# Kernel optimization log

Measured on AMD Instinct MI355X. Metric: run time of the kernel, lower is better.

## Reference

```python
import jax, jax.numpy as jnp
import numpy as np
import math

HIDDEN = 1024

def setup_inputs() -> dict:
    key = jax.random.key(0)
    k1, k2, k3, k4, k5 = jax.random.split(key, 5)
    s = 1.0 / math.sqrt(HIDDEN)
    return {
        "x": jax.random.normal(k1, (4, 2048, HIDDEN), dtype=jnp.float32),
        "W_qkv": jax.random.uniform(k2, (HIDDEN, 3 * HIDDEN), jnp.float32, -s, s),
        "b_qkv": jax.random.uniform(k3, (3 * HIDDEN,), jnp.float32, -s, s),
        "W_out": jax.random.uniform(k4, (HIDDEN, HIDDEN), jnp.float32, -s, s),
        "b_out": jax.random.uniform(k5, (HIDDEN,), jnp.float32, -s, s),
    }

def reference(x, W_qkv, b_qkv, W_out, b_out):
    # fused QKV projection: [b, s, 3h]
    qkv = jnp.einsum("bsh,hd->bsd", x, W_qkv) + b_qkv
    q, k, v = jnp.split(qkv, 3, axis=-1)
    scale = 1.0 / math.sqrt(x.shape[-1])
    scores = jnp.einsum("bqh,bkh->bqk", q, k) * scale  # [b, s, s]
    attn = jax.nn.softmax(scores, axis=-1)
    out = jnp.einsum("bqk,bkh->bqh", attn, v)
    return jnp.einsum("bsh,hd->bsd", out, W_out) + b_out
```

## Files before the change

kernel.cpp:

```cpp
#include <hip/hip_runtime.h>
#include <cstdint>
#include <cstddef>


typedef __bf16 bf16;
typedef __bf16 bf16x8 __attribute__((ext_vector_type(8)));
typedef __bf16 bf16x4 __attribute__((ext_vector_type(4)));
typedef float  f32x4  __attribute__((ext_vector_type(4)));

#define THREADS 512
#define BM 256
#define BN 128
#define BK 64
#define UNIT 8192
#define BUFELS (3*UNIT)
#define NBUF 3

__device__ __forceinline__ void gload_lds16(const bf16* g, bf16* l) {
  __builtin_amdgcn_global_load_lds(
      (const __attribute__((address_space(1))) unsigned int*)g,
      (__attribute__((address_space(3))) unsigned int*)l,
      16, 0, 0);
}

__device__ __forceinline__ void stage_unit(const bf16* g0, long ld, bf16* ldsu, int tid) {
  const int wv = tid >> 6;
  #pragma unroll
  for (int j = 0; j < 2; ++j) {
    const int c = j * 512 + tid;
    const int r = c >> 3;
    const int sg = (c & 7) ^ (r & 7);
    const int cb = j * 512 + (wv << 6);
    gload_lds16(g0 + (long)r * ld + sg * 8, ldsu + (size_t)cb * 8);
  }
}

__device__ __forceinline__ bf16x8 rd_frag(const bf16* unitb, int r, int s) {
  return *(const bf16x8*)(unitb + (size_t)r * 64 + (size_t)((s ^ (r & 7)) * 8));
}

template <int MODE>
__device__ __forceinline__ void gemm_body(
    const bf16* __restrict__ A, long sAz, int lda,
    const bf16* __restrict__ B, long sBz, int ldb, int K,
    bf16* __restrict__ p0, long sCz,
    bf16* __restrict__ p1, bf16* __restrict__ p2,
    float* __restrict__ fout, const float* __restrict__ bias, float scale) {
  __shared__ bf16 lds[NBUF * BUFELS];
  const int tid = threadIdx.x;
  const int wv = tid >> 6, ln = tid & 63;
  const int wr = wv >> 1, wc = wv & 1;
  const int lr = ln & 15, lh = ln >> 4;
  const int m0 = blockIdx.x * BM, n0 = blockIdx.y * BN;
  const int z = blockIdx.z;
  A += (long)z * sAz;
  B += (long)z * sBz;
  const bf16* Ag = A + (long)m0 * lda;
  const bf16* Bg = B + (long)n0 * ldb;
  const int NT = K / BK;

  #pragma unroll
  for (int t = 0; t < 2; ++t) {
    bf16* bb = lds + t * BUFELS;
    stage_unit(Ag + t * BK, lda, bb, tid);
    stage_unit(Ag + (long)128 * lda + t * BK, lda, bb + UNIT, tid);
    stage_unit(Bg + t * BK, ldb, bb + 2 * UNIT, tid);
  }
  asm volatile("s_waitcnt vmcnt(6)" ::: "memory");
  __builtin_amdgcn_sched_barrier(0);
  __builtin_amdgcn_s_barrier();

  f32x4 acc[4][4];
  #pragma unroll
  for (int i = 0; i < 4; ++i)
    #pragma unroll
    for (int j = 0; j < 4; ++j)
      acc[i][j] = f32x4{0.f, 0.f, 0.f, 0.f};

  const int aru = (wr & 1) * 64;
  const int au  = wr >> 1;

  int buf = 0, nb = 2;
  for (int t = 0; t < NT; ++t) {
    const bf16* Au = lds + buf * BUFELS + au * UNIT;
    const bf16* Bu = lds + buf * BUFELS + 2 * UNIT;
    bf16* Pn = lds + nb * BUFELS;
    const bool pf = (t + 2 < NT);
    bf16x8 aF[2][2], bF[4][2];

    #pragma unroll
    for (int i = 0; i < 2; ++i)
      #pragma unroll
      for (int ks = 0; ks < 2; ++ks)
        aF[i][ks] = rd_frag(Au, aru + i * 16 + lr, (ks << 2) + lh);
    #pragma unroll
    for (int nf = 0; nf < 4; ++nf)
      #pragma unroll
      for (int ks = 0; ks < 2; ++ks)
        bF[nf][ks] = rd_frag(Bu, wc * 64 + nf * 16 + lr, (ks << 2) + lh);
    if (pf) {
      stage_unit(Ag + (long)(t + 2) * BK, lda, Pn, tid);
      stage_unit(Ag + (long)128 * lda + (long)(t + 2) * BK, lda, Pn + UNIT, tid);
    }
    __builtin_amdgcn_s_barrier();
    asm volatile("s_waitcnt lgkmcnt(0)" ::: "memory");
    __builtin_amdgcn_sched_barrier(0);
    __builtin_amdgcn_s_setprio(1);
    #pragma unroll
    for (int i = 0; i < 2; ++i)
      #pragma unroll
      for (int nf = 0; nf < 4; ++nf)
        #pragma unroll
        for (int ks = 0; ks < 2; ++ks)
          acc[i][nf] = __builtin_amdgcn_mfma_f32_16x16x32_bf16(aF[i][ks], bF[nf][ks], acc[i][nf], 0, 0, 0);
    __builtin_amdgcn_s_setprio(0);
    __builtin_amdgcn_s_barrier();

    #pragma unroll
    for (int i = 0; i < 2; ++i)
      #pragma unroll
      for (int ks = 0; ks < 2; ++ks)
        aF[i][ks] = rd_frag(Au, aru + 32 + i * 16 + lr, (ks << 2) + lh);
    if (pf) stage_unit(Bg + (long)(t + 2) * BK, ldb, Pn + 2 * UNIT, tid);
    __builtin_amdgcn_s_barrier();
    asm volatile("s_waitcnt lgkmcnt(0)" ::: "memory");
    __builtin_amdgcn_sched_barrier(0);
    __builtin_amdgcn_s_setprio(1);
    #pragma unroll
    for (int i = 0; i < 2; ++i)
      #pragma unroll
      for (int nf = 0; nf < 4; ++nf)
        #pragma unroll
        for (int ks = 0; ks < 2; ++ks)
          acc[2 + i][nf] = __builtin_amdgcn_mfma_f32_16x16x32_bf16(aF[i][ks], bF[nf][ks], acc[2 + i][nf], 0, 0, 0);
    __builtin_amdgcn_s_setprio(0);
    if (t + 1 < NT) {
      if (pf) asm volatile("s_waitcnt vmcnt(6)" ::: "memory");
      else    asm volatile("s_waitcnt vmcnt(0)" ::: "memory");
      __builtin_amdgcn_sched_barrier(0);
    }
    __builtin_amdgcn_s_barrier();

    buf = (buf == 2) ? 0 : buf + 1;
    nb  = (nb == 2) ? 0 : nb + 1;
  }

  #pragma unroll
  for (int mf = 0; mf < 4; ++mf) {
    #pragma unroll
    for (int nf = 0; nf < 4; ++nf) {
      #pragma unroll
      for (int rg = 0; rg < 4; ++rg) {
        const int gm = m0 + wr * 64 + mf * 16 + lh * 4 + rg;
        const int gn = n0 + wc * 64 + nf * 16 + lr;
        float v = acc[mf][nf][rg];
        if constexpr (MODE == 0) {
          v += bias[gn];
          if (gn < 1024)       p0[(size_t)gm * 1024 + gn] = (bf16)v;
          else if (gn < 2048)  p1[(size_t)gm * 1024 + (gn - 1024)] = (bf16)v;
          else                 p2[(size_t)gm * 1024 + (gn - 2048)] = (bf16)v;
        } else if constexpr (MODE == 1) {
          p0[(size_t)z * sCz + (size_t)gm * 2048 + gn] = (bf16)(v * scale);
        } else if constexpr (MODE == 2) {
          p0[(size_t)z * sCz + (size_t)gm * 1024 + gn] = (bf16)v;
        } else {
          fout[(size_t)gm * 1024 + gn] = v + bias[gn];
        }
      }
    }
  }
}

#define GEMM_ARGS const bf16* A, long sAz, int lda, const bf16* B, long sBz, int ldb, \
                  int K, bf16* p0, long sCz, bf16* p1, bf16* p2, float* fout,         \
                  const float* bias, float scale
__global__ __launch_bounds__(THREADS, 2) void gemm_qkv(GEMM_ARGS) {
  gemm_body<0>(A, sAz, lda, B, sBz, ldb, K, p0, sCz, p1, p2, fout, bias, scale);
}
__global__ __launch_bounds__(THREADS, 2) void gemm_sc(GEMM_ARGS) {
  gemm_body<1>(A, sAz, lda, B, sBz, ldb, K, p0, sCz, p1, p2, fout, bias, scale);
}
__global__ __launch_bounds__(THREADS, 2) void gemm_pv(GEMM_ARGS) {
  gemm_body<2>(A, sAz, lda, B, sBz, ldb, K, p0, sCz, p1, p2, fout, bias, scale);
}
__global__ __launch_bounds__(THREADS, 2) void gemm_out(GEMM_ARGS) {
  gemm_body<3>(A, sAz, lda, B, sBz, ldb, K, p0, sCz, p1, p2, fout, bias, scale);
}

__global__ __launch_bounds__(256) void k_f32_to_bf16(const float* __restrict__ in,
                                                     bf16* __restrict__ out, long n) {
  long i = ((long)blockIdx.x * blockDim.x + threadIdx.x) * 4;
  if (i + 3 < n) {
    float4 v = *(const float4*)(in + i);
    bf16x4 o;
    o[0] = (bf16)v.x; o[1] = (bf16)v.y; o[2] = (bf16)v.z; o[3] = (bf16)v.w;
    *(bf16x4*)(out + i) = o;
  }
}

__global__ __launch_bounds__(256) void k_transpose(const float* __restrict__ in,
                                                   bf16* __restrict__ out, int R, int C) {
  __shared__ float t[32][33];
  int c0 = blockIdx.x * 32, r0 = blockIdx.y * 32;
  int tx = threadIdx.x, ty = threadIdx.y;
  #pragma unroll
  for (int dy = 0; dy < 32; dy += 8)
    t[ty + dy][tx] = in[(size_t)(r0 + ty + dy) * C + c0 + tx];
  __syncthreads();
  #pragma unroll
  for (int dy = 0; dy < 32; dy += 8)
    out[(size_t)(c0 + ty + dy) * R + r0 + tx] = (bf16)t[tx][ty + dy];
}

__global__ __launch_bounds__(256) void k_transpose_v(const bf16* __restrict__ in,
                                                     bf16* __restrict__ out) {
  __shared__ bf16 t[32][33];
  const int z = blockIdx.z;
  in  += (size_t)z * 2048 * 1024;
  out += (size_t)z * 1024 * 2048;
  int h0 = blockIdx.x * 32, s0 = blockIdx.y * 32;
  int tx = threadIdx.x, ty = threadIdx.y;
  #pragma unroll
  for (int dy = 0; dy < 32; dy += 8)
    t[ty + dy][tx] = in[(size_t)(s0 + ty + dy) * 1024 + h0 + tx];
  __syncthreads();
  #pragma unroll
  for (int dy = 0; dy < 32; dy += 8)
    out[(size_t)(h0 + ty + dy) * 2048 + s0 + tx] = t[tx][ty + dy];
}

__global__ __launch_bounds__(256) void k_softmax(bf16* __restrict__ S) {
  const int row = blockIdx.x;
  bf16* p = S + (size_t)row * 2048;
  const int tid = threadIdx.x;
  bf16x8 vin = *(const bf16x8*)(p + tid * 8);
  float x[8];
  float mx = -1e30f;
  #pragma unroll
  for (int i = 0; i < 8; ++i) { x[i] = (float)vin[i]; mx = fmaxf(mx, x[i]); }
  #pragma unroll
  for (int off = 32; off; off >>= 1) mx = fmaxf(mx, __shfl_down(mx, off));
  __shared__ float redm[4];
  if ((tid & 63) == 0) redm[tid >> 6] = mx;
  __syncthreads();
  mx = fmaxf(fmaxf(redm[0], redm[1]), fmaxf(redm[2], redm[3]));
  float s = 0.f;
  #pragma unroll
  for (int i = 0; i < 8; ++i) { x[i] = __expf(x[i] - mx); s += x[i]; }
  #pragma unroll
  for (int off = 32; off; off >>= 1) s += __shfl_down(s, off);
  __shared__ float reds[4];
  if ((tid & 63) == 0) reds[tid >> 6] = s;
  __syncthreads();
  s = reds[0] + reds[1] + reds[2] + reds[3];
  float inv = 1.0f / s;
  bf16x8 vo;
  #pragma unroll
  for (int i = 0; i < 8; ++i) vo[i] = (bf16)(x[i] * inv);
  *(bf16x8*)(p + tid * 8) = vo;
}

extern "C" void kernel_launch(void* const* d_in, const int* in_sizes, int n_in,
                              void* d_out, int out_size, void* d_ws, size_t ws_size,
                              hipStream_t stream) {
  const float* x    = (const float*)d_in[0];
  const float* Wqkv = (const float*)d_in[1];
  const float* bqkv = (const float*)d_in[2];
  const float* Wout = (const float*)d_in[3];
  const float* bout = (const float*)d_in[4];
  float* out = (float*)d_out;

  char* w = (char*)d_ws;
  const size_t MB = 1ull << 20;
  bf16* Xb  = (bf16*)(w);
  bf16* WqT = (bf16*)(w + 16 * MB);
  bf16* WoT = (bf16*)(w + 22 * MB);
  bf16* Qb  = (bf16*)(w + 24 * MB);
  bf16* Kb  = (bf16*)(w + 40 * MB);
  bf16* Vb  = (bf16*)(w + 56 * MB);
  bf16* Sb  = (bf16*)(w + 72 * MB);
  bf16* AO  = (bf16*)(w + 104 * MB);
  bf16* VT  = Xb;

  k_f32_to_bf16<<<8192, 256, 0, stream>>>(x, Xb, 8388608L);
  dim3 tb(32, 8);
  k_transpose<<<dim3(96, 32), tb, 0, stream>>>(Wqkv, WqT, 1024, 3072);
  k_transpose<<<dim3(32, 32), tb, 0, stream>>>(Wout, WoT, 1024, 1024);

  gemm_qkv<<<dim3(32, 24), THREADS, 0, stream>>>(
      Xb, 0L, 1024, WqT, 0L, 1024, 1024, Qb, 0L, Kb, Vb, nullptr, bqkv, 1.0f);

  k_transpose_v<<<dim3(32, 64, 4), tb, 0, stream>>>(Vb, VT);

  gemm_sc<<<dim3(8, 16, 4), THREADS, 0, stream>>>(
      Qb, 2048L * 1024, 1024, Kb, 2048L * 1024, 1024, 1024,
      Sb, 2048L * 2048, nullptr, nullptr, nullptr, nullptr, 0.03125f);

  k_softmax<<<8192, 256, 0, stream>>>(Sb);

  gemm_pv<<<dim3(8, 8, 4), THREADS, 0, stream>>>(
      Sb, 2048L * 2048, 2048, VT, 1024L * 2048, 2048, 2048,
      AO, 2048L * 1024, nullptr, nullptr, nullptr, nullptr, 1.0f);

  gemm_out<<<dim3(32, 8), THREADS, 0, stream>>>(
      AO, 0L, 1024, WoT, 0L, 1024, 1024,
      nullptr, 0L, nullptr, nullptr, out, bout, 1.0f);
}
```

Before: 227.2 us.

## Use 256x256 GEMM tiles with 8-phase double-buffered pipeline and XCD block swizzle

Grows the shared GEMM tile from 256x128 to 256x256 with a 2x4 wave layout and a 32-fragment accumulator per wave. The K loop becomes eight phases over two 64-wide LDS buffers, each quarter-unit prefetch staged between fragment reads and MFMAs with tuned vmcnt gates. Blocks are remapped with a stride-8 swizzle so neighbouring tiles land on the same XCD. The aim is more data reuse per LDS load and better L2 locality, at the cost of more registers, fewer blocks (worse wave fill on small grids like gemm_out) and fragile wait-count bookkeeping.

```diff
diff --git a/kernel.cpp b/kernel.cpp
--- a/kernel.cpp
+++ b/kernel.cpp
@@ -10,17 +10,13 @@
 
 #define THREADS 512
 #define BM 256
-#define BN 128
-#define BK 64
+#define BN 256
 #define UNIT 8192
-#define BUFELS (3*UNIT)
-#define NBUF 3
 
 __device__ __forceinline__ void gload_lds16(const bf16* g, bf16* l) {
   __builtin_amdgcn_global_load_lds(
       (const __attribute__((address_space(1))) unsigned int*)g,
-      (__attribute__((address_space(3))) unsigned int*)l,
-      16, 0, 0);
+      (__attribute__((address_space(3))) unsigned int*)l, 16, 0, 0);
 }
 
 __device__ __forceinline__ void stage_unit(const bf16* g0, long ld, bf16* ldsu, int tid) {
@@ -39,121 +35,120 @@
   return *(const bf16x8*)(unitb + (size_t)r * 64 + (size_t)((s ^ (r & 7)) * 8));
 }
 
+#define GATE(N)  asm volatile("s_waitcnt vmcnt(" #N ")" ::: "memory")
+#define LGKM0()  asm volatile("s_waitcnt lgkmcnt(0)" ::: "memory")
+#define SBAR()   __builtin_amdgcn_s_barrier()
+#define SCHED0() __builtin_amdgcn_sched_barrier(0)
+
+#define PHASE(DB, MH, NH, RA, RB, STAGE_CODE, GATE_CODE)                         \
+  {                                                                              \
+    if (RA) {                                                                    \
+      _Pragma("unroll") for (int mf = 0; mf < 4; ++mf)                           \
+        _Pragma("unroll") for (int ks = 0; ks < 2; ++ks)                         \
+          aF[mf][ks] = rd_frag(&lds[DB][MH][0], wsm * 64 + mf * 16 + lr, ks * 4 + lh); \
+    }                                                                            \
+    if (RB) {                                                                    \
+      _Pragma("unroll") for (int nf = 0; nf < 2; ++nf)                           \
+        _Pragma("unroll") for (int ks = 0; ks < 2; ++ks)                         \
+          bF[NH][nf][ks] = rd_frag(&lds[DB][2 + NH][0], wsn * 32 + nf * 16 + lr, ks * 4 + lh); \
+    }                                                                            \
+    STAGE_CODE;                                                                  \
+    SBAR();                                                                      \
+    LGKM0();                                                                     \
+    SCHED0();                                                                    \
+    __builtin_amdgcn_s_setprio(1);                                               \
+    _Pragma("unroll") for (int mf = 0; mf < 4; ++mf)                             \
+      _Pragma("unroll") for (int nf = 0; nf < 2; ++nf)                           \
+        _Pragma("unroll") for (int ks = 0; ks < 2; ++ks)                         \
+          acc[(MH)*4 + mf][(NH)*2 + nf] = __builtin_amdgcn_mfma_f32_16x16x32_bf16( \
+              aF[mf][ks], bF[NH][nf][ks], acc[(MH)*4 + mf][(NH)*2 + nf], 0, 0, 0); \
+    __builtin_amdgcn_s_setprio(0);                                               \
+    GATE_CODE;                                                                   \
+    SBAR();                                                                      \
+    SCHED0();                                                                    \
+  }
+
 template <int MODE>
 __device__ __forceinline__ void gemm_body(
     const bf16* __restrict__ A, long sAz, int lda,
     const bf16* __restrict__ B, long sBz, int ldb, int K,
-    bf16* __restrict__ p0, long sCz,
-    bf16* __restrict__ p1, bf16* __restrict__ p2,
+    bf16* __restrict__ p0, long sCz, bf16* __restrict__ p1, bf16* __restrict__ p2,
     float* __restrict__ fout, const float* __restrict__ bias, float scale) {
-  __shared__ bf16 lds[NBUF * BUFELS];
+  __shared__ bf16 lds[2][4][UNIT];
   const int tid = threadIdx.x;
   const int wv = tid >> 6, ln = tid & 63;
-  const int wr = wv >> 1, wc = wv & 1;
+  const int wsm = wv >> 2, wsn = wv & 3;
   const int lr = ln & 15, lh = ln >> 4;
-  const int m0 = blockIdx.x * BM, n0 = blockIdx.y * BN;
-  const int z = blockIdx.z;
-  A += (long)z * sAz;
-  B += (long)z * sBz;
-  const bf16* Ag = A + (long)m0 * lda;
-  const bf16* Bg = B + (long)n0 * ldb;
-  const int NT = K / BK;
-
-  #pragma unroll
-  for (int t = 0; t < 2; ++t) {
-    bf16* bb = lds + t * BUFELS;
-    stage_unit(Ag + t * BK, lda, bb, tid);
-    stage_unit(Ag + (long)128 * lda + t * BK, lda, bb + UNIT, tid);
-    stage_unit(Bg + t * BK, ldb, bb + 2 * UNIT, tid);
-  }
-  asm volatile("s_waitcnt vmcnt(6)" ::: "memory");
-  __builtin_amdgcn_sched_barrier(0);
-  __builtin_amdgcn_s_barrier();
-
-  f32x4 acc[4][4];
-  #pragma unroll
-  for (int i = 0; i < 4; ++i)
+
+  const int gx = gridDim.x, gy = gridDim.y;
+  const int lin = blockIdx.x + gx * (blockIdx.y + gy * blockIdx.z);
+  const int nwg = gx * gy * gridDim.z;
+  const int swz = (lin & 7) * (nwg >> 3) + (lin >> 3);
+  const int bx = swz % gx;
+  const int tq = swz / gx;
+  const int by = tq % gy;
+  const int z  = tq / gy;
+
+  const int m0 = bx * BM, n0 = by * BN;
+  const bf16* Ag = A + (long)z * sAz + (long)m0 * lda;
+  const bf16* Bg = B + (long)z * sBz + (long)n0 * ldb;
+  const int NITER = K / 128;
+
+  stage_unit(Ag,             lda, &lds[0][0][0], tid);
+  stage_unit(Bg,             ldb, &lds[0][2][0], tid);
+  stage_unit(Ag + 128 * lda, lda, &lds[0][1][0], tid);
+  stage_unit(Bg + 128 * ldb, ldb, &lds[0][3][0], tid);
+  stage_unit(Ag + 64,        lda, &lds[1][0][0], tid);
+  stage_unit(Bg + 64,        ldb, &lds[1][2][0], tid);
+  GATE(8);
+  SBAR();
+  SCHED0();
+
+  f32x4 acc[8][4];
+  #pragma unroll
+  for (int i = 0; i < 8; ++i)
     #pragma unroll
-    for (int j = 0; j < 4; ++j)
-      acc[i][j] = f32x4{0.f, 0.f, 0.f, 0.f};
-
-  const int aru = (wr & 1) * 64;
-  const int au  = wr >> 1;
-
-  int buf = 0, nb = 2;
-  for (int t = 0; t < NT; ++t) {
-    const bf16* Au = lds + buf * BUFELS + au * UNIT;
-    const bf16* Bu = lds + buf * BUFELS + 2 * UNIT;
-    bf16* Pn = lds + nb * BUFELS;
-    const bool pf = (t + 2 < NT);
-    bf16x8 aF[2][2], bF[4][2];
-
+    for (int j = 0; j < 4; ++j) acc[i][j] = f32x4{0.f, 0.f, 0.f, 0.f};
+  bf16x8 aF[4][2], bF[2][2][2];
+
+  for (int it = 0; it < NITER; ++it) {
+    const bool nl = (it + 1 < NITER);
+    const long ktA = 2L * it + 1, ktB = 2L * it + 2, ktC = 2L * it + 3;
+    PHASE(0, 0, 0, 1, 1,
+      { stage_unit(Ag + 128 * lda + ktA * 64, lda, &lds[1][1][0], tid); },
+      { GATE(6); });
+    PHASE(0, 0, 1, 0, 1,
+      { stage_unit(Bg + 128 * ldb + ktA * 64, ldb, &lds[1][3][0], tid); },
+      { GATE(10); });
+    PHASE(0, 1, 0, 1, 0,
+      { if (nl) stage_unit(Ag + ktB * 64, lda, &lds[0][0][0], tid); },
+      {});
+    PHASE(0, 1, 1, 0, 0,
+      { if (nl) stage_unit(Bg + ktB * 64, ldb, &lds[0][2][0], tid); },
+      { if (nl) { GATE(8); } else { GATE(4); } });
+    PHASE(1, 0, 0, 1, 1,
+      { if (nl) stage_unit(Ag + 128 * lda + ktB * 64, lda, &lds[0][1][0], tid); },
+      { if (nl) { GATE(6); } else { GATE(0); } });
+    PHASE(1, 0, 1, 0, 1,
+      { if (nl) stage_unit(Bg + 128 * ldb + ktB * 64, ldb, &lds[0][3][0], tid); },
+      { GATE(10); });
+    PHASE(1, 1, 0, 1, 0,
+      { if (nl) stage_unit(Ag + ktC * 64, lda, &lds[1][0][0], tid); },
+      {});
+    PHASE(1, 1, 1, 0, 0,
+      { if (nl) stage_unit(Bg + ktC * 64, ldb, &lds[1][2][0], tid); },
+      { GATE(8); });
+  }
+
+  #pragma unroll
+  for (int mi = 0; mi < 8; ++mi) {
     #pragma unroll
-    for (int i = 0; i < 2; ++i)
-      #pragma unroll
-      for (int ks = 0; ks < 2; ++ks)
-        aF[i][ks] = rd_frag(Au, aru + i * 16 + lr, (ks << 2) + lh);
-    #pragma unroll
-    for (int nf = 0; nf < 4; ++nf)
-      #pragma unroll
-      for (int ks = 0; ks < 2; ++ks)
-        bF[nf][ks] = rd_frag(Bu, wc * 64 + nf * 16 + lr, (ks << 2) + lh);
-    if (pf) {
-      stage_unit(Ag + (long)(t + 2) * BK, lda, Pn, tid);
-      stage_unit(Ag + (long)128 * lda + (long)(t + 2) * BK, lda, Pn + UNIT, tid);
-    }
-    __builtin_amdgcn_s_barrier();
-    asm volatile("s_waitcnt lgkmcnt(0)" ::: "memory");
-    __builtin_amdgcn_sched_barrier(0);
-    __builtin_amdgcn_s_setprio(1);
-    #pragma unroll
-    for (int i = 0; i < 2; ++i)
-      #pragma unroll
-      for (int nf = 0; nf < 4; ++nf)
-        #pragma unroll
-        for (int ks = 0; ks < 2; ++ks)
-          acc[i][nf] = __builtin_amdgcn_mfma_f32_16x16x32_bf16(aF[i][ks], bF[nf][ks], acc[i][nf], 0, 0, 0);
-    __builtin_amdgcn_s_setprio(0);
-    __builtin_amdgcn_s_barrier();
-
-    #pragma unroll
-    for (int i = 0; i < 2; ++i)
-      #pragma unroll
-      for (int ks = 0; ks < 2; ++ks)
-        aF[i][ks] = rd_frag(Au, aru + 32 + i * 16 + lr, (ks << 2) + lh);
-    if (pf) stage_unit(Bg + (long)(t + 2) * BK, ldb, Pn + 2 * UNIT, tid);
-    __builtin_amdgcn_s_barrier();
-    asm volatile("s_waitcnt lgkmcnt(0)" ::: "memory");
-    __builtin_amdgcn_sched_barrier(0);
-    __builtin_amdgcn_s_setprio(1);
-    #pragma unroll
-    for (int i = 0; i < 2; ++i)
-      #pragma unroll
-      for (int nf = 0; nf < 4; ++nf)
-        #pragma unroll
-        for (int ks = 0; ks < 2; ++ks)
-          acc[2 + i][nf] = __builtin_amdgcn_mfma_f32_16x16x32_bf16(aF[i][ks], bF[nf][ks], acc[2 + i][nf], 0, 0, 0);
-    __builtin_amdgcn_s_setprio(0);
-    if (t + 1 < NT) {
-      if (pf) asm volatile("s_waitcnt vmcnt(6)" ::: "memory");
-      else    asm volatile("s_waitcnt vmcnt(0)" ::: "memory");
-      __builtin_amdgcn_sched_barrier(0);
-    }
-    __builtin_amdgcn_s_barrier();
-
-    buf = (buf == 2) ? 0 : buf + 1;
-    nb  = (nb == 2) ? 0 : nb + 1;
-  }
-
-  #pragma unroll
-  for (int mf = 0; mf < 4; ++mf) {
-    #pragma unroll
-    for (int nf = 0; nf < 4; ++nf) {
+    for (int ni = 0; ni < 4; ++ni) {
       #pragma unroll
       for (int rg = 0; rg < 4; ++rg) {
-        const int gm = m0 + wr * 64 + mf * 16 + lh * 4 + rg;
-        const int gn = n0 + wc * 64 + nf * 16 + lr;
-        float v = acc[mf][nf][rg];
+        const int gm = m0 + (mi >> 2) * 128 + wsm * 64 + (mi & 3) * 16 + lh * 4 + rg;
+        const int gn = n0 + (ni >> 1) * 128 + wsn * 32 + (ni & 1) * 16 + lr;
+        float v = acc[mi][ni][rg];
         if constexpr (MODE == 0) {
           v += bias[gn];
           if (gn < 1024)       p0[(size_t)gm * 1024 + gn] = (bf16)v;
@@ -287,22 +282,22 @@
   k_transpose<<<dim3(96, 32), tb, 0, stream>>>(Wqkv, WqT, 1024, 3072);
   k_transpose<<<dim3(32, 32), tb, 0, stream>>>(Wout, WoT, 1024, 1024);
 
-  gemm_qkv<<<dim3(32, 24), THREADS, 0, stream>>>(
+  gemm_qkv<<<dim3(32, 12), THREADS, 0, stream>>>(
       Xb, 0L, 1024, WqT, 0L, 1024, 1024, Qb, 0L, Kb, Vb, nullptr, bqkv, 1.0f);
 
   k_transpose_v<<<dim3(32, 64, 4), tb, 0, stream>>>(Vb, VT);
 
-  gemm_sc<<<dim3(8, 16, 4), THREADS, 0, stream>>>(
+  gemm_sc<<<dim3(8, 8, 4), THREADS, 0, stream>>>(
       Qb, 2048L * 1024, 1024, Kb, 2048L * 1024, 1024, 1024,
       Sb, 2048L * 2048, nullptr, nullptr, nullptr, nullptr, 0.03125f);
 
   k_softmax<<<8192, 256, 0, stream>>>(Sb);
 
-  gemm_pv<<<dim3(8, 8, 4), THREADS, 0, stream>>>(
+  gemm_pv<<<dim3(8, 4, 4), THREADS, 0, stream>>>(
       Sb, 2048L * 2048, 2048, VT, 1024L * 2048, 2048, 2048,
       AO, 2048L * 1024, nullptr, nullptr, nullptr, nullptr, 1.0f);
 
-  gemm_out<<<dim3(32, 8), THREADS, 0, stream>>>(
+  gemm_out<<<dim3(32, 4), THREADS, 0, stream>>>(
       AO, 0L, 1024, WoT, 0L, 1024, 1024,
       nullptr, 0L, nullptr, nullptr, out, bout, 1.0f);
 }
```

After: 245.7 us. 1.08x slower.
